# Kernel optimization log

Hardware: AMD Instinct MI355X
Metric: run time of the kernel (lower is better)

The kernel has to match this reference:

```python
import jax, jax.numpy as jnp
import numpy as np

B, L, H, HEADS, BLOCKS = 4, 256, 256, 4, 2
D = H // HEADS
EPS = 1e-8
NEG = -4294967295.0  # -2**32 + 1


def rmsnorm(x, w):
    return x * jax.lax.rsqrt(jnp.mean(x * x, axis=-1, keepdims=True) + EPS) * w


def split_heads(x):  # [B,L,H] -> [h,B,L,d]
    return x.reshape(B, L, HEADS, D).transpose(2, 0, 1, 3)


def split_heads_tm(x):  # [B,L,L,H] -> [h,B,L,L,d]
    return x.reshape(B, L, L, HEADS, D).transpose(3, 0, 1, 2, 4)


def setup_inputs() -> dict:
    key = jax.random.key(0)
    ks = jax.random.split(key, 24)
    s = 0.02
    inp = {
        "seqs": jax.random.normal(ks[0], (B, L, H), jnp.float32),
        "attention_mask": jnp.triu(jnp.ones((L, L), jnp.bool_), k=1),  # causal: True = masked
        "timeline_mask": jnp.zeros((B, L), jnp.bool_),
        "time_matrix_K": jax.random.normal(ks[1], (B, L, L, H), jnp.float32),
        "time_matrix_V": jax.random.normal(ks[2], (B, L, L, H), jnp.float32),
        "abs_pos_K": jax.random.normal(ks[3], (B, L, H), jnp.float32),
        "abs_pos_V": jax.random.normal(ks[4], (B, L, H), jnp.float32),
        # parameters, stacked over blocks
        "ln_attn": jnp.ones((BLOCKS, H), jnp.float32),
        "Qw": jax.random.normal(ks[5], (BLOCKS, H, H), jnp.float32) * s,
        "Qb": jnp.zeros((BLOCKS, H), jnp.float32),
        "Kw": jax.random.normal(ks[6], (BLOCKS, H, H), jnp.float32) * s,
        "Kb": jnp.zeros((BLOCKS, H), jnp.float32),
        "Vw": jax.random.normal(ks[7], (BLOCKS, H, H), jnp.float32) * s,
        "Vb": jnp.zeros((BLOCKS, H), jnp.float32),
        "ln_ffn": jnp.ones((BLOCKS, H), jnp.float32),
        "W1": jax.random.normal(ks[8], (BLOCKS, H, H), jnp.float32) * s,
        "b1": jnp.zeros((BLOCKS, H), jnp.float32),
        "W2": jax.random.normal(ks[9], (BLOCKS, H, H), jnp.float32) * s,
        "b2": jnp.zeros((BLOCKS, H), jnp.float32),
        "ln_last": jnp.ones((H,), jnp.float32),
    }
    return inp


def reference(seqs, attention_mask, timeline_mask, time_matrix_K, time_matrix_V,
              abs_pos_K, abs_pos_V, ln_attn, Qw, Qb, Kw, Kb, Vw, Vb,
              ln_ffn, W1, b1, W2, b2, ln_last):
    tmK = split_heads_tm(time_matrix_K)           # [h,B,L,L,d]
    tmV = split_heads_tm(time_matrix_V)
    apK = split_heads(abs_pos_K)                  # [h,B,L,d]
    apV = split_heads(abs_pos_V)
    # True = masked; time_mask masks padded query rows, attn_mask is causal
    mask = timeline_mask[None, :, :, None] | attention_mask[None, None, :, :]  # [1,B,L,L]
    scale = 1.0 / jnp.sqrt(jnp.float32(D))
    not_pad = 1.0 - timeline_mask.astype(seqs.dtype)[:, :, None]  # [B,L,1]

    for i in range(BLOCKS):
        x = rmsnorm(seqs, ln_attn[i])
        Q = split_heads(x @ Qw[i].T + Qb[i])      # queries from normed x
        K = split_heads(seqs @ Kw[i].T + Kb[i])   # keys/values from raw seqs
        V = split_heads(seqs @ Vw[i].T + Vb[i])
        w = jnp.einsum('hbqd,hbkd->hbqk', Q, K)
        w += jnp.einsum('hbqd,hbkd->hbqk', Q, apK)
        w += jnp.einsum('hbqkd,hbqd->hbqk', tmK, Q)
        w = jnp.where(mask, NEG, w * scale)
        A = jax.nn.softmax(w, axis=-1)            # [h,B,L,L]
        out = jnp.einsum('hbqk,hbkd->hbqd', A, V)
        out += jnp.einsum('hbqk,hbkd->hbqd', A, apV)
        out += jnp.einsum('hbqk,hbqkd->hbqd', A, tmV)
        out = out.transpose(1, 2, 0, 3).reshape(B, L, H)  # merge heads
        seqs = seqs + out
        h2 = rmsnorm(seqs, ln_ffn[i])
        ffn = jax.nn.relu(h2 @ W1[i].T + b1[i]) @ W2[i].T + b2[i]
        seqs = (seqs + ffn) * not_pad
    return rmsnorm(seqs, ln_last)
```

## Files before the change

kernel.cpp:

```cpp
#include <hip/hip_runtime.h>
#include <math.h>

#define LLEN 256
#define HDIM 256
#define MM 1024
#define NEGV -4294967295.0f

__device__ __forceinline__ void gemm_core(
    float* A_s, float* W_s, float* r_s,
    const float* __restrict__ A, const float* __restrict__ ln,
    const float* __restrict__ W, const float* __restrict__ bias,
    const float* __restrict__ addv, const float* __restrict__ resid,
    const unsigned char* __restrict__ tl, float* __restrict__ C,
    int relu, int m0, int n0)
{
    int t = threadIdx.x;
    int tm = t >> 4, tn = t & 15;
    float acc[4][4];
    #pragma unroll
    for (int i = 0; i < 4; ++i)
        #pragma unroll
        for (int j = 0; j < 4; ++j) acc[i][j] = 0.f;
    float ssq[4] = {0.f, 0.f, 0.f, 0.f};

    for (int kc = 0; kc < HDIM; kc += 64) {
        #pragma unroll
        for (int i = 0; i < 4; ++i) {
            int idx = t + 256 * i;
            int row = idx >> 4, c4 = idx & 15;
            float4 v = *(const float4*)&A[(size_t)(m0 + row) * HDIM + kc + c4 * 4];
            ssq[i] += v.x * v.x + v.y * v.y + v.z * v.z + v.w * v.w;
            if (ln) {
                v.x *= ln[kc + c4 * 4 + 0]; v.y *= ln[kc + c4 * 4 + 1];
                v.z *= ln[kc + c4 * 4 + 2]; v.w *= ln[kc + c4 * 4 + 3];
            }
            *(float4*)&A_s[row * 68 + c4 * 4] = v;
        }
        #pragma unroll
        for (int i = 0; i < 4; ++i) {
            int idx = t + 256 * i;
            int row = idx >> 4, c4 = idx & 15;
            *(float4*)&W_s[row * 68 + c4 * 4] =
                *(const float4*)&W[(size_t)(n0 + row) * HDIM + kc + c4 * 4];
        }
        __syncthreads();
        #pragma unroll
        for (int k4 = 0; k4 < 16; ++k4) {
            float4 a[4], w[4];
            #pragma unroll
            for (int i = 0; i < 4; ++i)
                a[i] = *(const float4*)&A_s[(tm * 4 + i) * 68 + k4 * 4];
            #pragma unroll
            for (int j = 0; j < 4; ++j)
                w[j] = *(const float4*)&W_s[(tn * 4 + j) * 68 + k4 * 4];
            #pragma unroll
            for (int i = 0; i < 4; ++i)
                #pragma unroll
                for (int j = 0; j < 4; ++j)
                    acc[i][j] = fmaf(a[i].x, w[j].x, fmaf(a[i].y, w[j].y,
                                fmaf(a[i].z, w[j].z, fmaf(a[i].w, w[j].w, acc[i][j]))));
        }
        __syncthreads();
    }

    if (ln) {
        #pragma unroll
        for (int i = 0; i < 4; ++i) {
            float v = ssq[i];
            v += __shfl_xor(v, 1); v += __shfl_xor(v, 2);
            v += __shfl_xor(v, 4); v += __shfl_xor(v, 8);
            if (tn == 0) r_s[tm + 16 * i] = rsqrtf(v * (1.0f / HDIM) + 1e-8f);
        }
        __syncthreads();
    }

    float4 bv = *(const float4*)&bias[n0 + tn * 4];
    #pragma unroll
    for (int mm = 0; mm < 4; ++mm) {
        int row = m0 + tm * 4 + mm;
        float rr = ln ? r_s[tm * 4 + mm] : 1.0f;
        float tlf = tl ? (tl[row] ? 0.f : 1.f) : 1.f;
        float4 v;
        v.x = acc[mm][0] * rr + bv.x; v.y = acc[mm][1] * rr + bv.y;
        v.z = acc[mm][2] * rr + bv.z; v.w = acc[mm][3] * rr + bv.w;
        if (relu) {
            v.x = fmaxf(v.x, 0.f); v.y = fmaxf(v.y, 0.f);
            v.z = fmaxf(v.z, 0.f); v.w = fmaxf(v.w, 0.f);
        }
        size_t base = (size_t)row * HDIM + n0 + tn * 4;
        if (addv) {
            float4 o = *(const float4*)&addv[base];
            v.x += o.x; v.y += o.y; v.z += o.z; v.w += o.w;
        }
        if (resid) {
            float4 o = *(const float4*)&resid[base];
            v.x += o.x; v.y += o.y; v.z += o.z; v.w += o.w;
        }
        v.x *= tlf; v.y *= tlf; v.z *= tlf; v.w *= tlf;
        *(float4*)&C[base] = v;
    }
}

__global__ __launch_bounds__(256) void qkv_kernel(
    const float* __restrict__ s, const float* __restrict__ ln_attn,
    const float* __restrict__ Qw, const float* __restrict__ Qb,
    const float* __restrict__ Kw, const float* __restrict__ Kb,
    const float* __restrict__ Vw, const float* __restrict__ Vb,
    const float* __restrict__ apK, const float* __restrict__ apV,
    float* __restrict__ qb, float* __restrict__ kb, float* __restrict__ vb)
{
    __shared__ __align__(16) float A_s[64 * 68];
    __shared__ __align__(16) float W_s[64 * 68];
    __shared__ float r_s[64];
    int m0 = blockIdx.x * 64;
    int sel = blockIdx.y >> 2;
    int n0 = (blockIdx.y & 3) * 64;
    if (sel == 0)
        gemm_core(A_s, W_s, r_s, s, ln_attn, Qw, Qb, nullptr, nullptr, nullptr, qb, 0, m0, n0);
    else if (sel == 1)
        gemm_core(A_s, W_s, r_s, s, nullptr, Kw, Kb, apK, nullptr, nullptr, kb, 0, m0, n0);
    else
        gemm_core(A_s, W_s, r_s, s, nullptr, Vw, Vb, apV, nullptr, nullptr, vb, 0, m0, n0);
}

__global__ __launch_bounds__(256) void gemm_kernel(
    const float* __restrict__ A, const float* __restrict__ ln,
    const float* __restrict__ W, const float* __restrict__ bias,
    const float* __restrict__ resid, const unsigned char* __restrict__ tl,
    float* __restrict__ C, int relu)
{
    __shared__ __align__(16) float A_s[64 * 68];
    __shared__ __align__(16) float W_s[64 * 68];
    __shared__ float r_s[64];
    gemm_core(A_s, W_s, r_s, A, ln, W, bias, nullptr, resid, tl, C, relu,
              blockIdx.x * 64, blockIdx.y * 64);
}

__global__ __launch_bounds__(512) void attn_kernel(
    const float* __restrict__ Q, const float* __restrict__ Kp,
    const float* __restrict__ Vp, const float* __restrict__ tmK,
    const float* __restrict__ tmV, const unsigned char* __restrict__ tl,
    float* __restrict__ s)
{
    int g = blockIdx.x;
    int b = g >> 7, p = g & 127;
    int tid = threadIdx.x;
    int w = tid >> 6, lane = tid & 63;
    int hh = lane >> 4;

    __shared__ float w_s[4][257];
    __shared__ __align__(16) float out_s[8][256];

    const float4* Kp4 = (const float4*)(Kp + (size_t)b * LLEN * HDIM);
    const float4* Vp4 = (const float4*)(Vp + (size_t)b * LLEN * HDIM);

    #pragma unroll
    for (int rr = 0; rr < 2; ++rr) {
        int q = rr ? (LLEN - 1 - p) : p;
        int bq = b * LLEN + q;
        float4 qf = ((const float4*)(Q + (size_t)bq * HDIM))[lane];
        bool tlq = tl[bq] != 0;
        int kmax = tlq ? (LLEN - 1) : q;

        const float4* tmK4 = (const float4*)(tmK + (size_t)bq * LLEN * HDIM);
        const float4* tmV4 = (const float4*)(tmV + (size_t)bq * LLEN * HDIM);

        for (int k = w; k <= kmax; k += 8) {
            float4 kv = Kp4[k * 64 + lane];
            float4 tv = tmK4[k * 64 + lane];
            float sc = qf.x * (kv.x + tv.x) + qf.y * (kv.y + tv.y)
                     + qf.z * (kv.z + tv.z) + qf.w * (kv.w + tv.w);
            sc += __shfl_xor(sc, 1);
            sc += __shfl_xor(sc, 2);
            sc += __shfl_xor(sc, 4);
            sc += __shfl_xor(sc, 8);
            if ((lane & 15) == 0) w_s[lane >> 4][k] = sc;
        }
        __syncthreads();

        if (w < 4) {
            int h = w;
            float v0 = w_s[h][lane],       v1 = w_s[h][lane + 64];
            float v2 = w_s[h][lane + 128], v3 = w_s[h][lane + 192];
            v0 = (tlq || (lane       > q)) ? NEGV : v0 * 0.125f;
            v1 = (tlq || (lane + 64  > q)) ? NEGV : v1 * 0.125f;
            v2 = (tlq || (lane + 128 > q)) ? NEGV : v2 * 0.125f;
            v3 = (tlq || (lane + 192 > q)) ? NEGV : v3 * 0.125f;
            float mx = fmaxf(fmaxf(v0, v1), fmaxf(v2, v3));
            #pragma unroll
            for (int m2 = 1; m2 < 64; m2 <<= 1) mx = fmaxf(mx, __shfl_xor(mx, m2));
            float e0 = __expf(v0 - mx), e1 = __expf(v1 - mx);
            float e2 = __expf(v2 - mx), e3 = __expf(v3 - mx);
            float sm = e0 + e1 + e2 + e3;
            #pragma unroll
            for (int m2 = 1; m2 < 64; m2 <<= 1) sm += __shfl_xor(sm, m2);
            float inv = 1.0f / sm;
            w_s[h][lane] = e0 * inv;       w_s[h][lane + 64] = e1 * inv;
            w_s[h][lane + 128] = e2 * inv; w_s[h][lane + 192] = e3 * inv;
        }
        __syncthreads();

        float4 acc = {0.f, 0.f, 0.f, 0.f};
        for (int k = w; k <= kmax; k += 8) {
            float a = w_s[hh][k];
            float4 vv = Vp4[k * 64 + lane];
            float4 tv = tmV4[k * 64 + lane];
            acc.x = fmaf(a, vv.x + tv.x, acc.x);
            acc.y = fmaf(a, vv.y + tv.y, acc.y);
            acc.z = fmaf(a, vv.z + tv.z, acc.z);
            acc.w = fmaf(a, vv.w + tv.w, acc.w);
        }
        *(float4*)&out_s[w][lane * 4] = acc;
        __syncthreads();

        if (tid < 256) {
            float pp = 0.f;
            #pragma unroll
            for (int j = 0; j < 8; ++j) pp += out_s[j][tid];
            s[(size_t)bq * HDIM + tid] += pp;
        }
    }
}

__global__ __launch_bounds__(256) void rmsnorm_kernel(
    const float* __restrict__ x, const float* __restrict__ w, float* __restrict__ y)
{
    int row = blockIdx.x;
    int tid = threadIdx.x;
    float v = x[(size_t)row * HDIM + tid];
    float ss = v * v;
    #pragma unroll
    for (int m = 1; m < 64; m <<= 1) ss += __shfl_xor(ss, m);
    __shared__ float red[4];
    if ((tid & 63) == 0) red[tid >> 6] = ss;
    __syncthreads();
    float tot = red[0] + red[1] + red[2] + red[3];
    float r = rsqrtf(tot * (1.0f / HDIM) + 1e-8f);
    y[(size_t)row * HDIM + tid] = v * r * w[tid];
}

extern "C" void kernel_launch(void* const* d_in, const int* in_sizes, int n_in,
                              void* d_out, int out_size, void* d_ws, size_t ws_size,
                              hipStream_t stream)
{
    const float* seqs = (const float*)d_in[0];
    const unsigned char* tl = (const unsigned char*)d_in[2];
    const float* tmK = (const float*)d_in[3];
    const float* tmV = (const float*)d_in[4];
    const float* apK = (const float*)d_in[5];
    const float* apV = (const float*)d_in[6];
    const float* ln_attn = (const float*)d_in[7];
    const float* Qw = (const float*)d_in[8];
    const float* Qb = (const float*)d_in[9];
    const float* Kw = (const float*)d_in[10];
    const float* Kb = (const float*)d_in[11];
    const float* Vw = (const float*)d_in[12];
    const float* Vb = (const float*)d_in[13];
    const float* ln_ffn = (const float*)d_in[14];
    const float* W1 = (const float*)d_in[15];
    const float* b1 = (const float*)d_in[16];
    const float* W2 = (const float*)d_in[17];
    const float* b2 = (const float*)d_in[18];
    const float* ln_last = (const float*)d_in[19];
    float* out = (float*)d_out;

    const size_t NROW = (size_t)MM * HDIM;
    float* s  = (float*)d_ws;
    float* qb = s  + NROW;
    float* kb = qb + NROW;
    float* vb = kb + NROW;
    float* tb = vb + NROW;

    hipMemcpyAsync(s, seqs, NROW * sizeof(float), hipMemcpyDeviceToDevice, stream);

    for (int i = 0; i < 2; ++i) {
        const float* Qwi = Qw + (size_t)i * HDIM * HDIM;
        const float* Kwi = Kw + (size_t)i * HDIM * HDIM;
        const float* Vwi = Vw + (size_t)i * HDIM * HDIM;
        const float* W1i = W1 + (size_t)i * HDIM * HDIM;
        const float* W2i = W2 + (size_t)i * HDIM * HDIM;

        qkv_kernel<<<dim3(16, 12), 256, 0, stream>>>(
            s, ln_attn + i * HDIM, Qwi, Qb + i * HDIM, Kwi, Kb + i * HDIM,
            Vwi, Vb + i * HDIM, apK, apV, qb, kb, vb);
        attn_kernel<<<512, 512, 0, stream>>>(qb, kb, vb, tmK, tmV, tl, s);
        gemm_kernel<<<dim3(16, 4), 256, 0, stream>>>(
            s, ln_ffn + i * HDIM, W1i, b1 + i * HDIM, nullptr, nullptr, tb, 1);
        gemm_kernel<<<dim3(16, 4), 256, 0, stream>>>(
            tb, nullptr, W2i, b2 + i * HDIM, s, tl, s, 0);
    }
    rmsnorm_kernel<<<MM, 256, 0, stream>>>(s, ln_last, out);
}
```

Baseline: 235.6 us.

## Split attention blocks per head pair and remap GEMM threads per wavefront

The attention kernel now launches twice as many 256-thread blocks, each handling two of the four heads (half of the hidden dimension) for a pair of query rows. The aim is more blocks and higher occupancy over the bandwidth-bound time-matrix streaming. The GEMM core is also remapped so each thread computes one output column over 16 rows, with A tiles read by broadcast from unpadded shared memory. This trades the 4x4 register tile for more shared-memory loads per FMA, and loads Q/K/V rows twice across the two head-halves.

Result: slower. 335.1 us (+42.3%).

```diff
diff --git a/kernel.cpp b/kernel.cpp
--- a/kernel.cpp
+++ b/kernel.cpp
@@ -15,50 +15,38 @@
     int relu, int m0, int n0)
 {
     int t = threadIdx.x;
-    int tm = t >> 4, tn = t & 15;
-    float acc[4][4];
+    int srow = t >> 4, sc4 = t & 15;
+    int w = t >> 6, lane = t & 63;
+    int wrow = w * 16;
+    float acc[16];
     #pragma unroll
-    for (int i = 0; i < 4; ++i)
-        #pragma unroll
-        for (int j = 0; j < 4; ++j) acc[i][j] = 0.f;
+    for (int i = 0; i < 16; ++i) acc[i] = 0.f;
     float ssq[4] = {0.f, 0.f, 0.f, 0.f};
 
     for (int kc = 0; kc < HDIM; kc += 64) {
         #pragma unroll
         for (int i = 0; i < 4; ++i) {
-            int idx = t + 256 * i;
-            int row = idx >> 4, c4 = idx & 15;
-            float4 v = *(const float4*)&A[(size_t)(m0 + row) * HDIM + kc + c4 * 4];
-            ssq[i] += v.x * v.x + v.y * v.y + v.z * v.z + v.w * v.w;
+            int row = srow + 16 * i;
+            float4 va = *(const float4*)&A[(size_t)(m0 + row) * HDIM + kc + sc4 * 4];
+            ssq[i] += va.x*va.x + va.y*va.y + va.z*va.z + va.w*va.w;
             if (ln) {
-                v.x *= ln[kc + c4 * 4 + 0]; v.y *= ln[kc + c4 * 4 + 1];
-                v.z *= ln[kc + c4 * 4 + 2]; v.w *= ln[kc + c4 * 4 + 3];
+                va.x *= ln[kc + sc4*4 + 0]; va.y *= ln[kc + sc4*4 + 1];
+                va.z *= ln[kc + sc4*4 + 2]; va.w *= ln[kc + sc4*4 + 3];
             }
-            *(float4*)&A_s[row * 68 + c4 * 4] = v;
-        }
-        #pragma unroll
-        for (int i = 0; i < 4; ++i) {
-            int idx = t + 256 * i;
-            int row = idx >> 4, c4 = idx & 15;
-            *(float4*)&W_s[row * 68 + c4 * 4] =
-                *(const float4*)&W[(size_t)(n0 + row) * HDIM + kc + c4 * 4];
-        }
-        __syncthreads();
-        #pragma unroll
+            *(float4*)&A_s[row * 64 + sc4 * 4] = va;
+            *(float4*)&W_s[row * 68 + sc4 * 4] =
+                *(const float4*)&W[(size_t)(n0 + row) * HDIM + kc + sc4 * 4];
+        }
+        __syncthreads();
+        #pragma unroll 4
         for (int k4 = 0; k4 < 16; ++k4) {
-            float4 a[4], w[4];
-            #pragma unroll
-            for (int i = 0; i < 4; ++i)
-                a[i] = *(const float4*)&A_s[(tm * 4 + i) * 68 + k4 * 4];
-            #pragma unroll
-            for (int j = 0; j < 4; ++j)
-                w[j] = *(const float4*)&W_s[(tn * 4 + j) * 68 + k4 * 4];
-            #pragma unroll
-            for (int i = 0; i < 4; ++i)
-                #pragma unroll
-                for (int j = 0; j < 4; ++j)
-                    acc[i][j] = fmaf(a[i].x, w[j].x, fmaf(a[i].y, w[j].y,
-                                fmaf(a[i].z, w[j].z, fmaf(a[i].w, w[j].w, acc[i][j]))));
+            float4 wv = *(const float4*)&W_s[lane * 68 + k4 * 4];
+            #pragma unroll
+            for (int r = 0; r < 16; ++r) {
+                float4 av = *(const float4*)&A_s[(wrow + r) * 64 + k4 * 4];
+                acc[r] = fmaf(av.x, wv.x, fmaf(av.y, wv.y,
+                         fmaf(av.z, wv.z, fmaf(av.w, wv.w, acc[r]))));
+            }
         }
         __syncthreads();
     }
@@ -69,35 +57,24 @@
             float v = ssq[i];
             v += __shfl_xor(v, 1); v += __shfl_xor(v, 2);
             v += __shfl_xor(v, 4); v += __shfl_xor(v, 8);
-            if (tn == 0) r_s[tm + 16 * i] = rsqrtf(v * (1.0f / HDIM) + 1e-8f);
-        }
-        __syncthreads();
-    }
-
-    float4 bv = *(const float4*)&bias[n0 + tn * 4];
+            if (sc4 == 0) r_s[srow + 16 * i] = rsqrtf(v * (1.0f / HDIM) + 1e-8f);
+        }
+        __syncthreads();
+    }
+
+    int col = n0 + lane;
+    float bn = bias[col];
     #pragma unroll
-    for (int mm = 0; mm < 4; ++mm) {
-        int row = m0 + tm * 4 + mm;
-        float rr = ln ? r_s[tm * 4 + mm] : 1.0f;
-        float tlf = tl ? (tl[row] ? 0.f : 1.f) : 1.f;
-        float4 v;
-        v.x = acc[mm][0] * rr + bv.x; v.y = acc[mm][1] * rr + bv.y;
-        v.z = acc[mm][2] * rr + bv.z; v.w = acc[mm][3] * rr + bv.w;
-        if (relu) {
-            v.x = fmaxf(v.x, 0.f); v.y = fmaxf(v.y, 0.f);
-            v.z = fmaxf(v.z, 0.f); v.w = fmaxf(v.w, 0.f);
-        }
-        size_t base = (size_t)row * HDIM + n0 + tn * 4;
-        if (addv) {
-            float4 o = *(const float4*)&addv[base];
-            v.x += o.x; v.y += o.y; v.z += o.z; v.w += o.w;
-        }
-        if (resid) {
-            float4 o = *(const float4*)&resid[base];
-            v.x += o.x; v.y += o.y; v.z += o.z; v.w += o.w;
-        }
-        v.x *= tlf; v.y *= tlf; v.z *= tlf; v.w *= tlf;
-        *(float4*)&C[base] = v;
+    for (int r = 0; r < 16; ++r) {
+        int row = m0 + wrow + r;
+        float rr = ln ? r_s[wrow + r] : 1.0f;
+        float v = acc[r] * rr + bn;
+        if (relu) v = fmaxf(v, 0.f);
+        size_t idx = (size_t)row * HDIM + col;
+        if (addv)  v += addv[idx];
+        if (resid) v += resid[idx];
+        if (tl)    v *= (tl[row] ? 0.f : 1.f);
+        C[idx] = v;
     }
 }
 
@@ -109,7 +86,7 @@
     const float* __restrict__ apK, const float* __restrict__ apV,
     float* __restrict__ qb, float* __restrict__ kb, float* __restrict__ vb)
 {
-    __shared__ __align__(16) float A_s[64 * 68];
+    __shared__ __align__(16) float A_s[64 * 64];
     __shared__ __align__(16) float W_s[64 * 68];
     __shared__ float r_s[64];
     int m0 = blockIdx.x * 64;
@@ -129,59 +106,60 @@
     const float* __restrict__ resid, const unsigned char* __restrict__ tl,
     float* __restrict__ C, int relu)
 {
-    __shared__ __align__(16) float A_s[64 * 68];
+    __shared__ __align__(16) float A_s[64 * 64];
     __shared__ __align__(16) float W_s[64 * 68];
     __shared__ float r_s[64];
     gemm_core(A_s, W_s, r_s, A, ln, W, bias, nullptr, resid, tl, C, relu,
               blockIdx.x * 64, blockIdx.y * 64);
 }
 
-__global__ __launch_bounds__(512) void attn_kernel(
+__global__ __launch_bounds__(256, 8) void attn_kernel(
     const float* __restrict__ Q, const float* __restrict__ Kp,
     const float* __restrict__ Vp, const float* __restrict__ tmK,
     const float* __restrict__ tmV, const unsigned char* __restrict__ tl,
     float* __restrict__ s)
 {
     int g = blockIdx.x;
-    int b = g >> 7, p = g & 127;
+    int b = g >> 8;
+    int p = (g >> 1) & 127;
+    int hh = g & 1;
     int tid = threadIdx.x;
     int w = tid >> 6, lane = tid & 63;
-    int hh = lane >> 4;
-
-    __shared__ float w_s[4][257];
-    __shared__ __align__(16) float out_s[8][256];
-
-    const float4* Kp4 = (const float4*)(Kp + (size_t)b * LLEN * HDIM);
-    const float4* Vp4 = (const float4*)(Vp + (size_t)b * LLEN * HDIM);
-
-    #pragma unroll
+    int half = lane >> 5, lp = lane & 31;
+    int hl = lp >> 4;
+
+    __shared__ float w_s[2][257];
+    __shared__ __align__(16) float out_s[8][128];
+
+    const float4* Kp4 = (const float4*)Kp + (size_t)b * 16384 + hh * 32;
+    const float4* Vp4 = (const float4*)Vp + (size_t)b * 16384 + hh * 32;
+
     for (int rr = 0; rr < 2; ++rr) {
-        int q = rr ? (LLEN - 1 - p) : p;
-        int bq = b * LLEN + q;
-        float4 qf = ((const float4*)(Q + (size_t)bq * HDIM))[lane];
+        int q = rr ? (255 - p) : p;
+        int bq = b * 256 + q;
+        float4 qf = ((const float4*)(Q + (size_t)bq * HDIM + hh * 128))[lp];
         bool tlq = tl[bq] != 0;
         int kmax = tlq ? (LLEN - 1) : q;
 
-        const float4* tmK4 = (const float4*)(tmK + (size_t)bq * LLEN * HDIM);
-        const float4* tmV4 = (const float4*)(tmV + (size_t)bq * LLEN * HDIM);
-
-        for (int k = w; k <= kmax; k += 8) {
-            float4 kv = Kp4[k * 64 + lane];
-            float4 tv = tmK4[k * 64 + lane];
+        const float4* tmK4 = (const float4*)tmK + (size_t)bq * 16384 + hh * 32;
+        const float4* tmV4 = (const float4*)tmV + (size_t)bq * 16384 + hh * 32;
+
+        for (int k = w * 2 + half; k <= kmax; k += 8) {
+            float4 kv = Kp4[k * 64 + lp];
+            float4 tv = tmK4[k * 64 + lp];
             float sc = qf.x * (kv.x + tv.x) + qf.y * (kv.y + tv.y)
                      + qf.z * (kv.z + tv.z) + qf.w * (kv.w + tv.w);
             sc += __shfl_xor(sc, 1);
             sc += __shfl_xor(sc, 2);
             sc += __shfl_xor(sc, 4);
             sc += __shfl_xor(sc, 8);
-            if ((lane & 15) == 0) w_s[lane >> 4][k] = sc;
-        }
-        __syncthreads();
-
-        if (w < 4) {
-            int h = w;
-            float v0 = w_s[h][lane],       v1 = w_s[h][lane + 64];
-            float v2 = w_s[h][lane + 128], v3 = w_s[h][lane + 192];
+            if ((lane & 15) == 0) w_s[hl][k] = sc;
+        }
+        __syncthreads();
+
+        if (w < 2) {
+            float v0 = w_s[w][lane],       v1 = w_s[w][lane + 64];
+            float v2 = w_s[w][lane + 128], v3 = w_s[w][lane + 192];
             v0 = (tlq || (lane       > q)) ? NEGV : v0 * 0.125f;
             v1 = (tlq || (lane + 64  > q)) ? NEGV : v1 * 0.125f;
             v2 = (tlq || (lane + 128 > q)) ? NEGV : v2 * 0.125f;
@@ -195,29 +173,29 @@
             #pragma unroll
             for (int m2 = 1; m2 < 64; m2 <<= 1) sm += __shfl_xor(sm, m2);
             float inv = 1.0f / sm;
-            w_s[h][lane] = e0 * inv;       w_s[h][lane + 64] = e1 * inv;
-            w_s[h][lane + 128] = e2 * inv; w_s[h][lane + 192] = e3 * inv;
+            w_s[w][lane] = e0 * inv;       w_s[w][lane + 64] = e1 * inv;
+            w_s[w][lane + 128] = e2 * inv; w_s[w][lane + 192] = e3 * inv;
         }
         __syncthreads();
 
         float4 acc = {0.f, 0.f, 0.f, 0.f};
-        for (int k = w; k <= kmax; k += 8) {
-            float a = w_s[hh][k];
-            float4 vv = Vp4[k * 64 + lane];
-            float4 tv = tmV4[k * 64 + lane];
+        for (int k = w * 2 + half; k <= kmax; k += 8) {
+            float a = w_s[hl][k];
+            float4 vv = Vp4[k * 64 + lp];
+            float4 tv = tmV4[k * 64 + lp];
             acc.x = fmaf(a, vv.x + tv.x, acc.x);
             acc.y = fmaf(a, vv.y + tv.y, acc.y);
             acc.z = fmaf(a, vv.z + tv.z, acc.z);
             acc.w = fmaf(a, vv.w + tv.w, acc.w);
         }
-        *(float4*)&out_s[w][lane * 4] = acc;
-        __syncthreads();
-
-        if (tid < 256) {
+        *(float4*)&out_s[w * 2 + half][lp * 4] = acc;
+        __syncthreads();
+
+        if (tid < 128) {
             float pp = 0.f;
             #pragma unroll
             for (int j = 0; j < 8; ++j) pp += out_s[j][tid];
-            s[(size_t)bq * HDIM + tid] += pp;
+            s[(size_t)bq * HDIM + hh * 128 + tid] += pp;
         }
     }
 }
@@ -283,7 +261,7 @@
         qkv_kernel<<<dim3(16, 12), 256, 0, stream>>>(
             s, ln_attn + i * HDIM, Qwi, Qb + i * HDIM, Kwi, Kb + i * HDIM,
             Vwi, Vb + i * HDIM, apK, apV, qb, kb, vb);
-        attn_kernel<<<512, 512, 0, stream>>>(qb, kb, vb, tmK, tmV, tl, s);
+        attn_kernel<<<1024, 256, 0, stream>>>(qb, kb, vb, tmK, tmV, tl, s);
         gemm_kernel<<<dim3(16, 4), 256, 0, stream>>>(
             s, ln_ffn + i * HDIM, W1i, b1 + i * HDIM, nullptr, nullptr, tb, 1);
         gemm_kernel<<<dim3(16, 4), 256, 0, stream>>>(
```
